# Optimization experiments

Hardware: AMD Instinct MI355X
Metric: run time of the kernel (lower is better)

The kernel has to match this reference:

```python
import jax, jax.numpy as jnp
import numpy as np
import math

PHI = (1 + math.sqrt(5)) / 2
TABLE_SIZE = 4096
TWO_PI = 2.0 * math.pi
_ang = np.arange(TABLE_SIZE, dtype=np.float32) * (TWO_PI / TABLE_SIZE)
SIN_T = jnp.asarray(np.sin(_ang))
COS_T = jnp.asarray(np.cos(_ang))


def lookup_sin_cos(theta):
    """LUT sin/cos with linear interpolation over a 4096-entry table on [0, 2pi)."""
    pos = (theta / TWO_PI % 1.0) * TABLE_SIZE
    i0f = jnp.floor(pos)
    frac = pos - i0f
    i0 = i0f.astype(jnp.int32) % TABLE_SIZE
    i1 = (i0 + 1) % TABLE_SIZE
    s = SIN_T[i0] * (1.0 - frac) + SIN_T[i1] * frac
    c = COS_T[i0] * (1.0 - frac) + COS_T[i1] * frac
    return s, c


def setup_inputs() -> dict:
    key = jax.random.key(0)
    ks = jax.random.split(key, 8)
    B, S, D, H = 2, 2048, 1024, 16
    dh = D // H
    return {
        "x": jax.random.normal(ks[0], (B, S, D), dtype=jnp.float32),
        "w_q": jax.random.normal(ks[1], (H, dh), dtype=jnp.float32) * 0.02,
        "b_q": jnp.zeros((H, dh), jnp.float32),
        "phi_q": jnp.full((H, dh), PHI, jnp.float32),
        "w_k": jax.random.normal(ks[2], (H, dh), dtype=jnp.float32) * 0.02,
        "b_k": jnp.zeros((H, dh), jnp.float32),
        "phi_k": jnp.full((H, dh), PHI, jnp.float32),
        "w_v": jax.random.normal(ks[3], (H, dh), dtype=jnp.float32) * 0.02,
        "b_v": jnp.zeros((H, dh), jnp.float32),
        "w_out": jax.random.normal(ks[4], (D,), dtype=jnp.float32) * 0.02,
        "b_out": jnp.zeros((D,), jnp.float32),
    }


def reference(x, w_q, b_q, phi_q, w_k, b_k, phi_k, w_v, b_v, w_out, b_out):
    B, S, D = x.shape
    H, dh = w_q.shape
    scale = math.sqrt(2 * dh)
    t = jnp.arange(S, dtype=x.dtype).reshape(1, S, 1, 1)
    xh = x.reshape(B, S, H, dh)

    theta_q = xh / (1.0 + jnp.abs(w_q)) + b_q + t * phi_q
    sin_q, cos_q = lookup_sin_cos(theta_q)
    Q = jnp.concatenate([cos_q, sin_q], axis=-1)  # (B,S,H,2dh)

    theta_k = xh / (1.0 + jnp.abs(w_k)) + b_k + t * phi_k
    sin_k, cos_k = lookup_sin_cos(theta_k)
    K = jnp.concatenate([cos_k, sin_k], axis=-1)  # (B,S,H,2dh)

    theta_v = xh / (1.0 + jnp.abs(w_v)) + b_v
    sin_v, cos_v = lookup_sin_cos(theta_v)
    V = cos_v + sin_v  # (B,S,H,dh)

    scores = jnp.einsum('bqhd,bkhd->bhqk', Q, K) / scale
    causal = jnp.triu(jnp.ones((S, S), dtype=bool), k=1)
    scores = jnp.where(causal, -jnp.inf, scores)
    attn = jax.nn.softmax(scores, axis=-1)
    out = jnp.einsum('bhqk,bkhd->bqhd', attn, V).reshape(B, S, D)

    theta_out = out / (1.0 + jnp.abs(w_out)) + b_out
    sin_o, cos_o = lookup_sin_cos(theta_out)
    return cos_o + sin_o
```

## Files before the change

### kernel.cpp

```cpp
#include <hip/hip_runtime.h>
#include <hip/hip_bf16.h>
#include <math.h>

#define BB 2
#define SS 2048
#define HH 16
#define DH 64
#define DQK 128
#define DD (HH*DH)
#define QSCALE 0.08838834764831845f

typedef _Float16 half8_t __attribute__((ext_vector_type(8)));
typedef float f32x4_t __attribute__((ext_vector_type(4)));
typedef float f32x4v __attribute__((ext_vector_type(4)));

__device__ __forceinline__ void fsincos(float th, float* sn, float* cs) {
  float rev = th * 0.15915494309189535f;
  rev -= floorf(rev);
  float ang = rev * 6.283185307179586f;
  *sn = __sinf(ang);
  *cs = __cosf(ang);
}

__global__ __launch_bounds__(256) void gen_qkv(
    const float* __restrict__ x,
    const float* __restrict__ wq, const float* __restrict__ bq,
    const float* __restrict__ phq,
    const float* __restrict__ wk, const float* __restrict__ bk,
    const float* __restrict__ phk,
    const float* __restrict__ wv, const float* __restrict__ bv,
    _Float16* __restrict__ Qd, _Float16* __restrict__ Kd, _Float16* __restrict__ Vtd)
{
  int stile = blockIdx.x & 31;
  int bh    = blockIdx.x >> 5;
  int b = bh >> 4, h = bh & 15;
  int t = threadIdx.x;
  int sl = t >> 2;
  int dq = (t & 3) << 4;
  int s  = stile * 64 + sl;

  __shared__ _Float16 Vl[64 * 65];

  const float* xr = x + (((size_t)b * SS + s) * HH + h) * DH + dq;
  float xv[16];
#pragma unroll
  for (int i = 0; i < 4; i++)
    *(f32x4v*)(&xv[i * 4]) = *(const f32x4v*)(xr + i * 4);

  float tv = (float)s;
  _Float16 qc[16], qs[16], kc[16], ks[16];
#pragma unroll
  for (int i = 0; i < 16; i++) {
    int d = dq + i;
    int hd = h * DH + d;
    {
      float th = xv[i] / (1.f + fabsf(wq[hd])) + bq[hd] + tv * phq[hd];
      float sn, cs; fsincos(th, &sn, &cs);
      qc[i] = (_Float16)(cs * QSCALE);
      qs[i] = (_Float16)(sn * QSCALE);
    }
    {
      float th = xv[i] / (1.f + fabsf(wk[hd])) + bk[hd] + tv * phk[hd];
      float sn, cs; fsincos(th, &sn, &cs);
      kc[i] = (_Float16)cs;
      ks[i] = (_Float16)sn;
    }
    {
      float th = xv[i] / (1.f + fabsf(wv[hd])) + bv[hd];
      float sn, cs; fsincos(th, &sn, &cs);
      Vl[d * 65 + sl] = (_Float16)(cs + sn);
    }
  }
  size_t qbase = ((size_t)bh * SS + s) * DQK;
#pragma unroll
  for (int i = 0; i < 2; i++) {
    *(half8_t*)(Qd + qbase + dq + i * 8)      = *(half8_t*)(&qc[i * 8]);
    *(half8_t*)(Qd + qbase + DH + dq + i * 8) = *(half8_t*)(&qs[i * 8]);
    *(half8_t*)(Kd + qbase + dq + i * 8)      = *(half8_t*)(&kc[i * 8]);
    *(half8_t*)(Kd + qbase + DH + dq + i * 8) = *(half8_t*)(&ks[i * 8]);
  }
  __syncthreads();
#pragma unroll
  for (int i = 0; i < 16; i++) {
    int dout = i * 4 + (t >> 6);
    Vtd[((size_t)bh * DH + dout) * SS + stile * 64 + (t & 63)] =
        Vl[dout * 65 + (t & 63)];
  }
}

__global__ __launch_bounds__(512) void flash_attn(
    const _Float16* __restrict__ Qd, const _Float16* __restrict__ Kd,
    const _Float16* __restrict__ Vtd,
    const float* __restrict__ wout, const float* __restrict__ bout,
    float* __restrict__ out)
{
  int j  = blockIdx.x & 15;
  int bh = blockIdx.x >> 4;
  int wave = threadIdx.x >> 6;
  int lane = threadIdx.x & 63;
  int lm = lane & 15, lq = lane >> 4;
  int g = wave >> 1;
  int h = wave & 1;

  __shared__ __align__(16) _Float16 Kl[64 * 136];
  __shared__ __align__(16) _Float16 Vl[64 * 72];
  __shared__ __align__(16) _Float16 Pl[8][16 * 40];

  const _Float16* Kb = Kd + (size_t)bh * SS * DQK;
  const _Float16* Vb = Vtd + (size_t)bh * DH * SS;

  for (int phase = 0; phase < 2; ++phase) {
    int qt = phase == 0 ? (31 - j) : j;
    int nch = qt + 1;
    int q0 = qt * 64;

    const _Float16* Qb = Qd + ((size_t)bh * SS + q0 + g * 16) * DQK;
    half8_t aq[4];
#pragma unroll
    for (int c = 0; c < 4; c++)
      aq[c] = *(const half8_t*)(Qb + lm * DQK + c * 32 + lq * 8);

    f32x4_t o[4];
#pragma unroll
    for (int nt = 0; nt < 4; nt++) o[nt] = (f32x4_t){0.f, 0.f, 0.f, 0.f};
    float l[4] = {0.f, 0.f, 0.f, 0.f};

    for (int kt = 0; kt < nch; ++kt) {
      int k0 = kt * 64;
      __syncthreads();
#pragma unroll
      for (int i = 0; i < 2; i++) {
        int seg = threadIdx.x + i * 512;
        int key = seg >> 4;
        int fo  = (seg & 15) * 8;
        *(half8_t*)(&Kl[key * 136 + fo]) =
            *(const half8_t*)(Kb + (size_t)(k0 + key) * DQK + fo);
      }
      {
        int dv = threadIdx.x >> 3;
        int ko = (threadIdx.x & 7) * 8;
        *(half8_t*)(&Vl[dv * 72 + ko]) =
            *(const half8_t*)(Vb + (size_t)dv * SS + k0 + ko);
      }
      __syncthreads();

      f32x4_t c0 = (f32x4_t){0.f, 0.f, 0.f, 0.f};
      f32x4_t c1 = (f32x4_t){0.f, 0.f, 0.f, 0.f};
#pragma unroll
      for (int c = 0; c < 4; c++) {
        half8_t b0 = *(const half8_t*)(&Kl[(h * 32 + lm) * 136 + c * 32 + lq * 8]);
        half8_t b1 = *(const half8_t*)(&Kl[(h * 32 + 16 + lm) * 136 + c * 32 + lq * 8]);
        c0 = __builtin_amdgcn_mfma_f32_16x16x32_f16(aq[c], b0, c0, 0, 0, 0);
        c1 = __builtin_amdgcn_mfma_f32_16x16x32_f16(aq[c], b1, c1, 0, 0, 0);
      }

      bool maskit = (kt == nch - 1);
      float p0[4], p1[4];
#pragma unroll
      for (int r = 0; r < 4; r++) {
        float s0 = c0[r] - 8.f;
        float s1 = c1[r] - 8.f;
        if (maskit) {
          int qrow = q0 + g * 16 + lq * 4 + r;
          if (k0 + h * 32 + lm > qrow)      s0 = -1e30f;
          if (k0 + h * 32 + 16 + lm > qrow) s1 = -1e30f;
        }
        p0[r] = __expf(s0);
        p1[r] = __expf(s1);
        l[r] += p0[r] + p1[r];
      }

      _Float16* pw = &Pl[wave][0];
#pragma unroll
      for (int r = 0; r < 4; r++) {
        pw[(lq * 4 + r) * 40 + lm]      = (_Float16)p0[r];
        pw[(lq * 4 + r) * 40 + 16 + lm] = (_Float16)p1[r];
      }
      half8_t pa = *(const half8_t*)(&pw[lm * 40 + lq * 8]);

#pragma unroll
      for (int nt = 0; nt < 4; nt++) {
        half8_t bv2 = *(const half8_t*)(&Vl[(nt * 16 + lm) * 72 + h * 32 + lq * 8]);
        o[nt] = __builtin_amdgcn_mfma_f32_16x16x32_f16(pa, bv2, o[nt], 0, 0, 0);
      }
    }

    float* Os = (float*)&Kl[0];
    float* Ls = (float*)&Vl[0];
    __syncthreads();
    if (h == 1) {
      float* dst = Os + ((size_t)g * 64 + lane) * 17;
#pragma unroll
      for (int nt = 0; nt < 4; nt++)
#pragma unroll
        for (int r = 0; r < 4; r++) dst[nt * 4 + r] = o[nt][r];
      float* dl = Ls + ((size_t)g * 64 + lane) * 5;
#pragma unroll
      for (int r = 0; r < 4; r++) dl[r] = l[r];
    }
    __syncthreads();
    if (h == 0) {
      const float* src = Os + ((size_t)g * 64 + lane) * 17;
#pragma unroll
      for (int nt = 0; nt < 4; nt++)
#pragma unroll
        for (int r = 0; r < 4; r++) o[nt][r] += src[nt * 4 + r];
      const float* sl = Ls + ((size_t)g * 64 + lane) * 5;
#pragma unroll
      for (int r = 0; r < 4; r++) l[r] += sl[r];
#pragma unroll
      for (int off = 1; off < 16; off <<= 1)
#pragma unroll
        for (int r = 0; r < 4; r++) l[r] += __shfl_xor(l[r], off);

      int b = bh >> 4, hh = bh & 15;
#pragma unroll
      for (int r = 0; r < 4; r++) {
        float rl = 1.f / l[r];
        int qrow = q0 + g * 16 + lq * 4 + r;
#pragma unroll
        for (int nt = 0; nt < 4; nt++) {
          int dcol = hh * DH + nt * 16 + lm;
          float ov = o[nt][r] * rl;
          float th = ov / (1.f + fabsf(wout[dcol])) + bout[dcol];
          float sn, cs; fsincos(th, &sn, &cs);
          out[((size_t)b * SS + qrow) * DD + dcol] = cs + sn;
        }
      }
    }
  }
}

extern "C" void kernel_launch(void* const* d_in, const int* in_sizes, int n_in,
                              void* d_out, int out_size, void* d_ws, size_t ws_size,
                              hipStream_t stream) {
  (void)in_sizes; (void)n_in; (void)out_size; (void)ws_size;
  const float* x   = (const float*)d_in[0];
  const float* wq  = (const float*)d_in[1];
  const float* bq  = (const float*)d_in[2];
  const float* phq = (const float*)d_in[3];
  const float* wk  = (const float*)d_in[4];
  const float* bk  = (const float*)d_in[5];
  const float* phk = (const float*)d_in[6];
  const float* wv  = (const float*)d_in[7];
  const float* bv  = (const float*)d_in[8];
  const float* wo  = (const float*)d_in[9];
  const float* bo  = (const float*)d_in[10];

  _Float16* Qd  = (_Float16*)d_ws;
  _Float16* Kd  = Qd + (size_t)BB * HH * SS * DQK;
  _Float16* Vtd = Kd + (size_t)BB * HH * SS * DQK;

  gen_qkv<<<BB * HH * (SS / 64), 256, 0, stream>>>(
      x, wq, bq, phq, wk, bk, phk, wv, bv, Qd, Kd, Vtd);
  flash_attn<<<BB * HH * 16, 512, 0, stream>>>(
      Qd, Kd, Vtd, wo, bo, (float*)d_out);
}
```

Before: 163.9 us.

## Double-buffer K/V via direct global-to-LDS loads with pre-swizzled tile layout

gen_qkv now writes K and V^T in a tiled, MFMA-fragment-friendly layout so each 64-key tile is one contiguous chunk. flash_attn uses global_load_lds DMA into a double-buffered LDS region, prefetching the next tile while the current one is computed, and drops to 256 threads with each wave covering 32 query rows (2 M-tiles) to reuse K/V fragments across more MFMAs. The aim is to hide global load latency and cut register staging and LDS traffic, at the cost of more registers per wave and fewer waves per block.

Result: slower. 169.0 us (+3.1%).

```diff
diff --git a/kernel.cpp b/kernel.cpp
--- a/kernel.cpp
+++ b/kernel.cpp
@@ -20,6 +20,12 @@
   float ang = rev * 6.283185307179586f;
   *sn = __sinf(ang);
   *cs = __cosf(ang);
+}
+
+__device__ __forceinline__ void dma16(const void* g, void* l) {
+  __builtin_amdgcn_global_load_lds(
+      (const __attribute__((address_space(1))) unsigned int*)g,
+      (__attribute__((address_space(3))) unsigned int*)l, 16, 0, 0);
 }
 
 __global__ __launch_bounds__(256) void gen_qkv(
@@ -76,19 +82,29 @@
   for (int i = 0; i < 2; i++) {
     *(half8_t*)(Qd + qbase + dq + i * 8)      = *(half8_t*)(&qc[i * 8]);
     *(half8_t*)(Qd + qbase + DH + dq + i * 8) = *(half8_t*)(&qs[i * 8]);
-    *(half8_t*)(Kd + qbase + dq + i * 8)      = *(half8_t*)(&kc[i * 8]);
-    *(half8_t*)(Kd + qbase + DH + dq + i * 8) = *(half8_t*)(&ks[i * 8]);
+  }
+  {
+    size_t ktb = ((size_t)bh * 32 + stile) * 8192;
+    int fo0 = (t & 3) * 2;
+    *(half8_t*)(Kd + ktb + ((size_t)(fo0    ) * 64 + sl) * 8) = *(half8_t*)(&kc[0]);
+    *(half8_t*)(Kd + ktb + ((size_t)(fo0 + 1) * 64 + sl) * 8) = *(half8_t*)(&kc[8]);
+    *(half8_t*)(Kd + ktb + ((size_t)(fo0 + 8) * 64 + sl) * 8) = *(half8_t*)(&ks[0]);
+    *(half8_t*)(Kd + ktb + ((size_t)(fo0 + 9) * 64 + sl) * 8) = *(half8_t*)(&ks[8]);
   }
   __syncthreads();
 #pragma unroll
-  for (int i = 0; i < 16; i++) {
-    int dout = i * 4 + (t >> 6);
-    Vtd[((size_t)bh * DH + dout) * SS + stile * 64 + (t & 63)] =
-        Vl[dout * 65 + (t & 63)];
-  }
-}
-
-__global__ __launch_bounds__(512) void flash_attn(
+  for (int i = 0; i < 2; i++) {
+    int u = t * 2 + i;
+    int dv = u & 63, ku = u >> 6;
+    _Float16 tmp[8];
+#pragma unroll
+    for (int jj = 0; jj < 8; jj++) tmp[jj] = Vl[dv * 65 + ku * 8 + jj];
+    *(half8_t*)(Vtd + (((size_t)bh * 32 + stile) * 8 + ku) * 512 + dv * 8) =
+        *(half8_t*)tmp;
+  }
+}
+
+__global__ __launch_bounds__(256) void flash_attn(
     const _Float16* __restrict__ Qd, const _Float16* __restrict__ Kd,
     const _Float16* __restrict__ Vtd,
     const float* __restrict__ wout, const float* __restrict__ bout,
@@ -99,134 +115,149 @@
   int wave = threadIdx.x >> 6;
   int lane = threadIdx.x & 63;
   int lm = lane & 15, lq = lane >> 4;
-  int g = wave >> 1;
-  int h = wave & 1;
-
-  __shared__ __align__(16) _Float16 Kl[64 * 136];
-  __shared__ __align__(16) _Float16 Vl[64 * 72];
-  __shared__ __align__(16) _Float16 Pl[8][16 * 40];
-
-  const _Float16* Kb = Kd + (size_t)bh * SS * DQK;
-  const _Float16* Vb = Vtd + (size_t)bh * DH * SS;
+  int qh = wave >> 1;
+  int kh = wave & 1;
+
+  __shared__ __align__(16) _Float16 KV[2][12288];
+  __shared__ __align__(16) _Float16 Pbuf[4][32 * 36];
+
+  const _Float16* Kg = Kd + (size_t)bh * 32 * 8192;
+  const _Float16* Vg = Vtd + (size_t)bh * 32 * 4096;
+  _Float16* Pw = &Pbuf[wave][0];
 
   for (int phase = 0; phase < 2; ++phase) {
     int qt = phase == 0 ? (31 - j) : j;
     int nch = qt + 1;
     int q0 = qt * 64;
 
-    const _Float16* Qb = Qd + ((size_t)bh * SS + q0 + g * 16) * DQK;
-    half8_t aq[4];
-#pragma unroll
-    for (int c = 0; c < 4; c++)
-      aq[c] = *(const half8_t*)(Qb + lm * DQK + c * 32 + lq * 8);
-
-    f32x4_t o[4];
-#pragma unroll
-    for (int nt = 0; nt < 4; nt++) o[nt] = (f32x4_t){0.f, 0.f, 0.f, 0.f};
-    float l[4] = {0.f, 0.f, 0.f, 0.f};
+    __syncthreads();
+
+    const _Float16* Qb = Qd + ((size_t)bh * SS + q0 + qh * 32) * DQK;
+    half8_t aq[2][4];
+#pragma unroll
+    for (int mt = 0; mt < 2; mt++)
+#pragma unroll
+      for (int c = 0; c < 4; c++)
+        aq[mt][c] = *(const half8_t*)(Qb + (mt * 16 + lm) * DQK + c * 32 + lq * 8);
+
+    f32x4_t o[2][4];
+    float l[2][4];
+#pragma unroll
+    for (int mt = 0; mt < 2; mt++) {
+#pragma unroll
+      for (int nt4 = 0; nt4 < 4; nt4++) o[mt][nt4] = (f32x4_t){0.f, 0.f, 0.f, 0.f};
+#pragma unroll
+      for (int r = 0; r < 4; r++) l[mt][r] = 0.f;
+    }
+
+    {
+#pragma unroll
+      for (int i = 0; i < 4; i++)
+        dma16(Kg + (size_t)(wave * 4 + i) * 512 + lane * 8, &KV[0][(wave * 4 + i) * 512]);
+#pragma unroll
+      for (int i = 0; i < 2; i++)
+        dma16(Vg + (size_t)(wave * 2 + i) * 512 + lane * 8, &KV[0][8192 + (wave * 2 + i) * 512]);
+    }
 
     for (int kt = 0; kt < nch; ++kt) {
+      int bf = kt & 1;
+      asm volatile("s_waitcnt vmcnt(0)" ::: "memory");
+      __syncthreads();
+      if (kt + 1 < nch) {
+        int nb = (kt + 1) & 1;
+        const _Float16* gK = Kg + (size_t)(kt + 1) * 8192;
+        const _Float16* gV = Vg + (size_t)(kt + 1) * 4096;
+#pragma unroll
+        for (int i = 0; i < 4; i++)
+          dma16(gK + (size_t)(wave * 4 + i) * 512 + lane * 8, &KV[nb][(wave * 4 + i) * 512]);
+#pragma unroll
+        for (int i = 0; i < 2; i++)
+          dma16(gV + (size_t)(wave * 2 + i) * 512 + lane * 8, &KV[nb][8192 + (wave * 2 + i) * 512]);
+      }
+
+      const _Float16* lK = &KV[bf][0];
+      const _Float16* lV = &KV[bf][8192];
       int k0 = kt * 64;
-      __syncthreads();
-#pragma unroll
-      for (int i = 0; i < 2; i++) {
-        int seg = threadIdx.x + i * 512;
-        int key = seg >> 4;
-        int fo  = (seg & 15) * 8;
-        *(half8_t*)(&Kl[key * 136 + fo]) =
-            *(const half8_t*)(Kb + (size_t)(k0 + key) * DQK + fo);
+
+      f32x4_t cS[2][2];
+      cS[0][0] = cS[0][1] = cS[1][0] = cS[1][1] = (f32x4_t){0.f, 0.f, 0.f, 0.f};
+#pragma unroll
+      for (int c = 0; c < 4; c++) {
+        int fo = c * 4 + lq;
+        half8_t b0 = *(const half8_t*)(lK + ((size_t)fo * 64 + kh * 32 + lm) * 8);
+        half8_t b1 = *(const half8_t*)(lK + ((size_t)fo * 64 + kh * 32 + 16 + lm) * 8);
+        cS[0][0] = __builtin_amdgcn_mfma_f32_16x16x32_f16(aq[0][c], b0, cS[0][0], 0, 0, 0);
+        cS[1][0] = __builtin_amdgcn_mfma_f32_16x16x32_f16(aq[1][c], b0, cS[1][0], 0, 0, 0);
+        cS[0][1] = __builtin_amdgcn_mfma_f32_16x16x32_f16(aq[0][c], b1, cS[0][1], 0, 0, 0);
+        cS[1][1] = __builtin_amdgcn_mfma_f32_16x16x32_f16(aq[1][c], b1, cS[1][1], 0, 0, 0);
       }
-      {
-        int dv = threadIdx.x >> 3;
-        int ko = (threadIdx.x & 7) * 8;
-        *(half8_t*)(&Vl[dv * 72 + ko]) =
-            *(const half8_t*)(Vb + (size_t)dv * SS + k0 + ko);
+
+      bool maskit = (kt == nch - 1);
+#pragma unroll
+      for (int mt = 0; mt < 2; mt++)
+#pragma unroll
+        for (int nt = 0; nt < 2; nt++)
+#pragma unroll
+          for (int r = 0; r < 4; r++) {
+            float sv = cS[mt][nt][r] - 8.f;
+            if (maskit) {
+              int qrow = q0 + qh * 32 + mt * 16 + lq * 4 + r;
+              int key  = k0 + kh * 32 + nt * 16 + lm;
+              if (key > qrow) sv = -1e30f;
+            }
+            float p = __expf(sv);
+            l[mt][r] += p;
+            Pw[(mt * 16 + lq * 4 + r) * 36 + nt * 16 + lm] = (_Float16)p;
+          }
+
+      half8_t pa0 = *(const half8_t*)(Pw + (lm) * 36 + lq * 8);
+      half8_t pa1 = *(const half8_t*)(Pw + (16 + lm) * 36 + lq * 8);
+#pragma unroll
+      for (int nt4 = 0; nt4 < 4; nt4++) {
+        half8_t bv2 = *(const half8_t*)(lV + ((size_t)(kh * 4 + lq) * 64 + nt4 * 16 + lm) * 8);
+        o[0][nt4] = __builtin_amdgcn_mfma_f32_16x16x32_f16(pa0, bv2, o[0][nt4], 0, 0, 0);
+        o[1][nt4] = __builtin_amdgcn_mfma_f32_16x16x32_f16(pa1, bv2, o[1][nt4], 0, 0, 0);
       }
-      __syncthreads();
-
-      f32x4_t c0 = (f32x4_t){0.f, 0.f, 0.f, 0.f};
-      f32x4_t c1 = (f32x4_t){0.f, 0.f, 0.f, 0.f};
-#pragma unroll
-      for (int c = 0; c < 4; c++) {
-        half8_t b0 = *(const half8_t*)(&Kl[(h * 32 + lm) * 136 + c * 32 + lq * 8]);
-        half8_t b1 = *(const half8_t*)(&Kl[(h * 32 + 16 + lm) * 136 + c * 32 + lq * 8]);
-        c0 = __builtin_amdgcn_mfma_f32_16x16x32_f16(aq[c], b0, c0, 0, 0, 0);
-        c1 = __builtin_amdgcn_mfma_f32_16x16x32_f16(aq[c], b1, c1, 0, 0, 0);
-      }
-
-      bool maskit = (kt == nch - 1);
-      float p0[4], p1[4];
-#pragma unroll
-      for (int r = 0; r < 4; r++) {
-        float s0 = c0[r] - 8.f;
-        float s1 = c1[r] - 8.f;
-        if (maskit) {
-          int qrow = q0 + g * 16 + lq * 4 + r;
-          if (k0 + h * 32 + lm > qrow)      s0 = -1e30f;
-          if (k0 + h * 32 + 16 + lm > qrow) s1 = -1e30f;
+    }
+
+    __syncthreads();
+    float* Of = (float*)&KV[0][0];
+    float* Lf = ((float*)&KV[0][0]) + 2 * 32 * 68;
+    if (kh == 1) {
+#pragma unroll
+      for (int mt = 0; mt < 2; mt++)
+#pragma unroll
+        for (int r = 0; r < 4; r++) {
+          int row = qh * 32 + mt * 16 + lq * 4 + r;
+          float* dst = Of + (size_t)row * 68;
+#pragma unroll
+          for (int nt4 = 0; nt4 < 4; nt4++) dst[nt4 * 16 + lm] = o[mt][nt4][r];
+          Lf[(size_t)row * 17 + lm] = l[mt][r];
         }
-        p0[r] = __expf(s0);
-        p1[r] = __expf(s1);
-        l[r] += p0[r] + p1[r];
-      }
-
-      _Float16* pw = &Pl[wave][0];
-#pragma unroll
-      for (int r = 0; r < 4; r++) {
-        pw[(lq * 4 + r) * 40 + lm]      = (_Float16)p0[r];
-        pw[(lq * 4 + r) * 40 + 16 + lm] = (_Float16)p1[r];
-      }
-      half8_t pa = *(const half8_t*)(&pw[lm * 40 + lq * 8]);
-
-#pragma unroll
-      for (int nt = 0; nt < 4; nt++) {
-        half8_t bv2 = *(const half8_t*)(&Vl[(nt * 16 + lm) * 72 + h * 32 + lq * 8]);
-        o[nt] = __builtin_amdgcn_mfma_f32_16x16x32_f16(pa, bv2, o[nt], 0, 0, 0);
-      }
-    }
-
-    float* Os = (float*)&Kl[0];
-    float* Ls = (float*)&Vl[0];
+    }
     __syncthreads();
-    if (h == 1) {
-      float* dst = Os + ((size_t)g * 64 + lane) * 17;
-#pragma unroll
-      for (int nt = 0; nt < 4; nt++)
-#pragma unroll
-        for (int r = 0; r < 4; r++) dst[nt * 4 + r] = o[nt][r];
-      float* dl = Ls + ((size_t)g * 64 + lane) * 5;
-#pragma unroll
-      for (int r = 0; r < 4; r++) dl[r] = l[r];
-    }
-    __syncthreads();
-    if (h == 0) {
-      const float* src = Os + ((size_t)g * 64 + lane) * 17;
-#pragma unroll
-      for (int nt = 0; nt < 4; nt++)
-#pragma unroll
-        for (int r = 0; r < 4; r++) o[nt][r] += src[nt * 4 + r];
-      const float* sl = Ls + ((size_t)g * 64 + lane) * 5;
-#pragma unroll
-      for (int r = 0; r < 4; r++) l[r] += sl[r];
-#pragma unroll
-      for (int off = 1; off < 16; off <<= 1)
-#pragma unroll
-        for (int r = 0; r < 4; r++) l[r] += __shfl_xor(l[r], off);
-
+    if (kh == 0) {
       int b = bh >> 4, hh = bh & 15;
 #pragma unroll
-      for (int r = 0; r < 4; r++) {
-        float rl = 1.f / l[r];
-        int qrow = q0 + g * 16 + lq * 4 + r;
-#pragma unroll
-        for (int nt = 0; nt < 4; nt++) {
-          int dcol = hh * DH + nt * 16 + lm;
-          float ov = o[nt][r] * rl;
-          float th = ov / (1.f + fabsf(wout[dcol])) + bout[dcol];
-          float sn, cs; fsincos(th, &sn, &cs);
-          out[((size_t)b * SS + qrow) * DD + dcol] = cs + sn;
+      for (int mt = 0; mt < 2; mt++)
+#pragma unroll
+        for (int r = 0; r < 4; r++) {
+          int row = qh * 32 + mt * 16 + lq * 4 + r;
+          const float* src = Of + (size_t)row * 68;
+          float lsum = l[mt][r] + Lf[(size_t)row * 17 + lm];
+#pragma unroll
+          for (int off = 1; off < 16; off <<= 1) lsum += __shfl_xor(lsum, off);
+          float rl = 1.f / lsum;
+          int qrow = q0 + row;
+#pragma unroll
+          for (int nt4 = 0; nt4 < 4; nt4++) {
+            float ov = (o[mt][nt4][r] + src[nt4 * 16 + lm]) * rl;
+            int dcol = hh * DH + nt4 * 16 + lm;
+            float th = ov / (1.f + fabsf(wout[dcol])) + bout[dcol];
+            float sn, cs; fsincos(th, &sn, &cs);
+            out[((size_t)b * SS + qrow) * DD + dcol] = cs + sn;
+          }
         }
-      }
     }
   }
 }
@@ -253,6 +284,6 @@
 
   gen_qkv<<<BB * HH * (SS / 64), 256, 0, stream>>>(
       x, wq, bq, phq, wk, bk, phk, wv, bv, Qd, Kd, Vtd);
-  flash_attn<<<BB * HH * 16, 512, 0, stream>>>(
+  flash_attn<<<BB * HH * 16, 256, 0, stream>>>(
       Qd, Kd, Vtd, wo, bo, (float*)d_out);
 }
```
